# Optimization experiments

Hardware: AMD Instinct MI355X
Metric: run time of the kernel (lower is better)

Reference implementation:

```python
import jax, jax.numpy as jnp
import numpy as np

B, N, IN_DIM, DIM, HEADS = 2, 4096, 1024, 1024, 8
MAX_MASK = 2048
SCALE = DIM ** -0.5  # original uses full dim, not per-head dim


def setup_inputs() -> dict:
    key = jax.random.key(0)
    k_x, k_qkv, k_o, k_b, k_m = jax.random.split(key, 5)
    x = jax.random.normal(k_x, (B, N, IN_DIM), dtype=jnp.float32)
    W_qkv = jax.random.normal(k_qkv, (IN_DIM, 3 * DIM), dtype=jnp.float32) * 0.02
    W_out = jax.random.normal(k_o, (DIM, DIM), dtype=jnp.float32) * 0.02
    b_out = jax.random.normal(k_b, (DIM,), dtype=jnp.float32) * 0.02
    mask = jax.random.randint(k_m, (1, 1, MAX_MASK, MAX_MASK), 0, 2, dtype=jnp.int32)
    return {"x": x, "W_qkv": W_qkv, "W_out": W_out, "b_out": b_out,
            "mask": mask, "max_mask": MAX_MASK}


def reference(x, W_qkv, W_out, b_out, mask, max_mask):
    b, n, _ = x.shape
    d = DIM // HEADS
    qkv = x @ W_qkv                                   # [b, n, 3*dim]
    qkv = qkv.reshape(b, n, 3, HEADS, d).transpose(2, 0, 3, 1, 4)  # [3, b, h, n, d]
    q, k, v = qkv[0], qkv[1], qkv[2]
    dots = jnp.einsum('bhid,bhjd->bhij', q, k) * SCALE  # [b, h, n, n]
    # partial submatrix masking on the top-left [max_mask, max_mask] block
    m = max_mask
    sub = jnp.where(mask == 0, -jnp.inf, dots[:, :, :m, :m])
    dots = dots.at[:, :, :m, :m].set(sub)
    attn = jax.nn.softmax(dots, axis=-1)
    out = jnp.einsum('bhij,bhjd->bhid', attn, v)       # [b, h, n, d]
    out = out.transpose(0, 2, 1, 3).reshape(b, n, HEADS * d)
    return out @ W_out + b_out
```

## Files before the change

kernel.cpp:

```cpp
#include <hip/hip_runtime.h>
#include <hip/hip_bf16.h>
#include <stdint.h>


typedef __attribute__((ext_vector_type(8))) short short8;
typedef __attribute__((ext_vector_type(4))) float f32x4;

#define SCALE_Q 0.03125f

__device__ __forceinline__ unsigned short f2bf(float f) {
  union { float f; unsigned int u; } v;
  v.f = f;
  return (unsigned short)((v.u + 0x7fffu + ((v.u >> 16) & 1u)) >> 16);
}

__device__ __forceinline__ unsigned int pkbf2(float a, float b) {
  __hip_bfloat162 h = __float22bfloat162_rn(make_float2(a, b));
  union { __hip_bfloat162 h; unsigned int u; } c;
  c.h = h;
  return c.u;
}

__device__ __forceinline__ void gload_lds16(const void* g, void* l) {
  __builtin_amdgcn_global_load_lds(
      (const __attribute__((address_space(1))) uint32_t*)(uintptr_t)g,
      (__attribute__((address_space(3))) uint32_t*)(uintptr_t)l, 16, 0, 0);
}

__device__ __forceinline__ f32x4 zero4() {
  f32x4 z; z.x = 0.f; z.y = 0.f; z.z = 0.f; z.w = 0.f; return z;
}

__global__ __launch_bounds__(256) void k_cvt_x(const float* __restrict__ in,
                                               unsigned short* __restrict__ out) {
  const int t = blockIdx.x * 256 + threadIdx.x;
  const float4 v = ((const float4*)in)[t];
  ushort4 o;
  o.x = f2bf(v.x); o.y = f2bf(v.y); o.z = f2bf(v.z); o.w = f2bf(v.w);
  ((ushort4*)out)[t] = o;
}

__global__ __launch_bounds__(256) void k_cvt_wt(const float* __restrict__ w,
                                                unsigned short* __restrict__ wt,
                                                int Nn) {
  __shared__ float t[32][33];
  const int n0 = blockIdx.x << 5, k0 = blockIdx.y << 5;
  const int c = threadIdx.x & 31, r8 = threadIdx.x >> 5;
#pragma unroll
  for (int i = 0; i < 4; ++i) {
    const int r = (i << 3) + r8;
    t[r][c] = w[(long)(k0 + r) * Nn + n0 + c];
  }
  __syncthreads();
#pragma unroll
  for (int i = 0; i < 4; ++i) {
    const int r = (i << 3) + r8;
    wt[(long)(n0 + r) * 1024 + k0 + c] = f2bf(t[c][r]);
  }
}

__global__ __launch_bounds__(256) void k_mask_bits(
    const int* __restrict__ m, unsigned long long* __restrict__ mb) {
  const int t = blockIdx.x * 256 + threadIdx.x;
  const unsigned long long b = __ballot(m[t] != 0);
  if ((threadIdx.x & 63) == 0) mb[t >> 6] = b;
}

__global__ __launch_bounds__(256, 2) void k_qkv_gemm(
    const unsigned short* __restrict__ A,
    const unsigned short* __restrict__ Bt,
    unsigned short* __restrict__ Qs, unsigned short* __restrict__ Ks,
    unsigned short* __restrict__ Vt) {
  __shared__ __align__(16) unsigned short lA[4][128][8];
  __shared__ __align__(16) unsigned short lB[4][128][8];
  const int tid = threadIdx.x;
  const int w = tid >> 6, ln = tid & 63;
  const int m15 = ln & 15, q4 = ln >> 4;
  const int wm = (w >> 1) << 6, wn = (w & 1) << 6;
  const int id = blockIdx.x;
  const int swz = (id & 7) * 192 + (id >> 3);
  const int tn = swz % 24, tm = swz / 24;
  const int which = tn >> 3;
  const int h = tn & 7;

  f32x4 acc[4][4];
#pragma unroll
  for (int i = 0; i < 4; ++i)
#pragma unroll
    for (int j = 0; j < 4; ++j) acc[i][j] = zero4();

  if (which == 2) {
    for (int kb = 0; kb < 1024; kb += 32) {
      __syncthreads();
#pragma unroll
      for (int c = 0; c < 2; ++c) {
        const int p = ((c * 4 + w) << 10) + (ln << 4);
        const int g = p >> 11;
        const int r = (p & 2047) >> 4;
        gload_lds16(A + ((long)tm * 128 + r) * 1024 + kb + g * 8,
                    (char*)&lA[0][0][0] + p);
        gload_lds16(Bt + ((long)tn * 128 + r) * 1024 + kb + g * 8,
                    (char*)&lB[0][0][0] + p);
      }
      __syncthreads();
      short8 afr[4], bfr[4];
#pragma unroll
      for (int i = 0; i < 4; ++i)
        afr[i] = *(const short8*)&lA[q4][wm + i * 16 + m15][0];
#pragma unroll
      for (int j = 0; j < 4; ++j)
        bfr[j] = *(const short8*)&lB[q4][wn + j * 16 + m15][0];
#pragma unroll
      for (int i = 0; i < 4; ++i)
#pragma unroll
        for (int j = 0; j < 4; ++j)
          acc[i][j] = __builtin_amdgcn_mfma_f32_16x16x32_bf16(afr[i], bfr[j],
                                                              acc[i][j], 0, 0, 0);
    }
#pragma unroll
    for (int i = 0; i < 4; ++i) {
      const int m0 = (tm << 7) + wm + (i << 4) + (q4 << 2);
      const int b = m0 >> 12, row0 = m0 & 4095;
#pragma unroll
      for (int j = 0; j < 4; ++j) {
        const int dd = wn + (j << 4) + m15;
        const long bh = b * 8 + h;
        uint2 u;
        u.x = pkbf2(acc[i][j][0], acc[i][j][1]);
        u.y = pkbf2(acc[i][j][2], acc[i][j][3]);
        *(uint2*)&Vt[(bh * 128 + dd) * 4096 + row0] = u;
      }
    }
  } else {
    for (int kb = 0; kb < 1024; kb += 32) {
      __syncthreads();
#pragma unroll
      for (int c = 0; c < 2; ++c) {
        const int p = ((c * 4 + w) << 10) + (ln << 4);
        const int g = p >> 11;
        const int r = (p & 2047) >> 4;
        gload_lds16(A + ((long)tm * 128 + r) * 1024 + kb + g * 8,
                    (char*)&lA[0][0][0] + p);
        gload_lds16(Bt + ((long)tn * 128 + r) * 1024 + kb + g * 8,
                    (char*)&lB[0][0][0] + p);
      }
      __syncthreads();
      short8 afr[4], bfr[4];
#pragma unroll
      for (int i = 0; i < 4; ++i)
        afr[i] = *(const short8*)&lA[q4][wm + i * 16 + m15][0];
#pragma unroll
      for (int j = 0; j < 4; ++j)
        bfr[j] = *(const short8*)&lB[q4][wn + j * 16 + m15][0];
#pragma unroll
      for (int i = 0; i < 4; ++i)
#pragma unroll
        for (int j = 0; j < 4; ++j)
          acc[i][j] = __builtin_amdgcn_mfma_f32_16x16x32_bf16(bfr[j], afr[i],
                                                              acc[i][j], 0, 0, 0);
    }
    unsigned short* Dst = (which == 0) ? Qs : Ks;
    const float sc = (which == 0) ? SCALE_Q : 1.0f;
#pragma unroll
    for (int i = 0; i < 4; ++i) {
      const int m = (tm << 7) + wm + (i << 4) + m15;
      const int b = m >> 12, row = m & 4095;
      const long bh = b * 8 + h;
#pragma unroll
      for (int j = 0; j < 4; ++j) {
        const int dd0 = wn + (j << 4) + (q4 << 2);
        uint2 u;
        u.x = pkbf2(acc[i][j][0] * sc, acc[i][j][1] * sc);
        u.y = pkbf2(acc[i][j][2] * sc, acc[i][j][3] * sc);
        *(uint2*)&Dst[(bh * 4096 + row) * 128 + dd0] = u;
      }
    }
  }
}

__global__ __launch_bounds__(512, 2) void k_flash(
    const unsigned short* __restrict__ Qs, const unsigned short* __restrict__ Ks,
    const unsigned short* __restrict__ Vt,
    const unsigned long long* __restrict__ mbits,
    unsigned short* __restrict__ Ob) {
  __shared__ __align__(16) unsigned short lK[2][16][64][8];
  __shared__ __align__(16) unsigned short lV[2][8][128][8];
  __shared__ __align__(16) unsigned short lP[8][2][16][72];

  const int tid = threadIdx.x;
  const int w = tid >> 6, ln = tid & 63;
  const int m15 = ln & 15, q4 = ln >> 4;
  const int id = blockIdx.x;
  const int xcd = id & 7, jj = id >> 3;
  const int bh = (xcd << 1) | (jj >> 4);
  const int rowblk = jj & 15;
  const int rbase = rowblk * 256 + w * 32;
  const int rq0 = rbase + m15;
  const int rq1 = rbase + 16 + m15;

  const unsigned short* Qbh = Qs + (long)bh * 524288;
  const unsigned short* Kbh = Ks + (long)bh * 524288;
  const unsigned short* Vbh = Vt + (long)bh * 524288;

  short8 qf[2][4];
#pragma unroll
  for (int kk = 0; kk < 4; ++kk) {
    qf[0][kk] = *(const short8*)(Qbh + (long)rq0 * 128 + kk * 32 + q4 * 8);
    qf[1][kk] = *(const short8*)(Qbh + (long)rq1 * 128 + kk * 32 + q4 * 8);
  }

  f32x4 o[2][8];
#pragma unroll
  for (int qg = 0; qg < 2; ++qg)
#pragma unroll
    for (int j = 0; j < 8; ++j) o[qg][j] = zero4();
  f32x4 lacc[2];
  lacc[0] = zero4(); lacc[1] = zero4();

  const bool maskblk = rowblk < 8;

#define STAGE_KV(dst, kvoff)                                              \
  {                                                                       \
    _Pragma("unroll")                                                     \
    for (int c = 0; c < 2; ++c) {                                         \
      const int p = ((c * 8 + w) << 10) + (ln << 4);                      \
      const int cs = p >> 10;                                             \
      const int j = (p & 1023) >> 4;                                      \
      gload_lds16(Kbh + (long)((kvoff) + j) * 128 + cs * 8,               \
                  (char*)&lK[dst][0][0][0] + p);                          \
    }                                                                     \
    _Pragma("unroll")                                                     \
    for (int c = 0; c < 2; ++c) {                                         \
      const int p = ((c * 8 + w) << 10) + (ln << 4);                      \
      const int cv = p >> 11;                                             \
      const int dv = (p & 2047) >> 4;                                     \
      gload_lds16(Vbh + (long)dv * 4096 + (kvoff) + cv * 8,               \
                  (char*)&lV[dst][0][0][0] + p);                          \
    }                                                                     \
  }

  STAGE_KV(0, 0);
  __syncthreads();

  int cur = 0;
  for (int kv = 0; kv < 4096; kv += 64) {
    unsigned long long mw0 = 0ull, mw1 = 0ull;
    const bool domask = maskblk && (kv < 2048);
    if (domask) {
      mw0 = mbits[(long)rq0 * 32 + (kv >> 6)];
      mw1 = mbits[(long)rq1 * 32 + (kv >> 6)];
    }

    const int nb = cur ^ 1;
    if (kv + 64 < 4096) STAGE_KV(nb, kv + 64);

    f32x4 s[2][4];
#pragma unroll
    for (int jt = 0; jt < 4; ++jt) { s[0][jt] = zero4(); s[1][jt] = zero4(); }
    __builtin_amdgcn_s_setprio(1);
#pragma unroll
    for (int jt = 0; jt < 4; ++jt) {
#pragma unroll
      for (int kk = 0; kk < 4; ++kk) {
        const short8 kfr = *(const short8*)&lK[cur][kk * 4 + q4][jt * 16 + m15][0];
        s[0][jt] = __builtin_amdgcn_mfma_f32_16x16x32_bf16(kfr, qf[0][kk],
                                                           s[0][jt], 0, 0, 0);
        s[1][jt] = __builtin_amdgcn_mfma_f32_16x16x32_bf16(kfr, qf[1][kk],
                                                           s[1][jt], 0, 0, 0);
      }
    }
    __builtin_amdgcn_s_setprio(0);

    if (domask) {
#pragma unroll
      for (int jt = 0; jt < 4; ++jt) {
        const unsigned int u0 =
            (jt & 2) ? (unsigned int)(mw0 >> 32) : (unsigned int)mw0;
        const unsigned int u1 =
            (jt & 2) ? (unsigned int)(mw1 >> 32) : (unsigned int)mw1;
        const int base = ((jt & 1) << 4) + (q4 << 2);
#pragma unroll
        for (int r = 0; r < 4; ++r) {
          if (!((u0 >> (base + r)) & 1u)) s[0][jt][r] = -1e30f;
          if (!((u1 >> (base + r)) & 1u)) s[1][jt][r] = -1e30f;
        }
      }
    }

#pragma unroll
    for (int jt = 0; jt < 4; ++jt) {
      f32x4 p0, p1;
      p0.x = __expf(s[0][jt].x); p0.y = __expf(s[0][jt].y);
      p0.z = __expf(s[0][jt].z); p0.w = __expf(s[0][jt].w);
      p1.x = __expf(s[1][jt].x); p1.y = __expf(s[1][jt].y);
      p1.z = __expf(s[1][jt].z); p1.w = __expf(s[1][jt].w);
      lacc[0] += p0; lacc[1] += p1;
      uint2 u0, u1;
      u0.x = pkbf2(p0.x, p0.y); u0.y = pkbf2(p0.z, p0.w);
      u1.x = pkbf2(p1.x, p1.y); u1.y = pkbf2(p1.z, p1.w);
      *(uint2*)&lP[w][0][m15][jt * 16 + q4 * 4] = u0;
      *(uint2*)&lP[w][1][m15][jt * 16 + q4 * 4] = u1;
    }
    __asm__ volatile("s_waitcnt lgkmcnt(0)" ::: "memory");
    __builtin_amdgcn_sched_barrier(0);

    __builtin_amdgcn_s_setprio(1);
#pragma unroll
    for (int kk2 = 0; kk2 < 2; ++kk2) {
      const short8 pf0 = *(const short8*)&lP[w][0][m15][kk2 * 32 + q4 * 8];
      const short8 pf1 = *(const short8*)&lP[w][1][m15][kk2 * 32 + q4 * 8];
#pragma unroll
      for (int jt2 = 0; jt2 < 8; ++jt2) {
        const short8 vf = *(const short8*)&lV[cur][kk2 * 4 + q4][jt2 * 16 + m15][0];
        o[0][jt2] = __builtin_amdgcn_mfma_f32_16x16x32_bf16(pf0, vf,
                                                            o[0][jt2], 0, 0, 0);
        o[1][jt2] = __builtin_amdgcn_mfma_f32_16x16x32_bf16(pf1, vf,
                                                            o[1][jt2], 0, 0, 0);
      }
    }
    __builtin_amdgcn_s_setprio(0);

    __syncthreads();
    cur = nb;
  }
#undef STAGE_KV

  const int b = bh >> 3, h = bh & 7;
#pragma unroll
  for (int qg = 0; qg < 2; ++qg) {
    float lh = lacc[qg].x + lacc[qg].y + lacc[qg].z + lacc[qg].w;
    lh += __shfl_xor(lh, 16);
    lh += __shfl_xor(lh, 32);
    const float linv = 1.0f / lh;
#pragma unroll
    for (int r = 0; r < 4; ++r) {
      const float li = __shfl(linv, q4 * 4 + r);
      const int row = rbase + qg * 16 + q4 * 4 + r;
      unsigned short* op = Ob + ((long)(b * 4096 + row)) * 1024 + h * 128;
#pragma unroll
      for (int jt2 = 0; jt2 < 8; ++jt2)
        op[jt2 * 16 + m15] = f2bf(o[qg][jt2][r] * li);
    }
  }
}

__global__ __launch_bounds__(256, 2) void k_proj_gemm(
    const unsigned short* __restrict__ A,
    const unsigned short* __restrict__ Bt,
    const float* __restrict__ bias, float* __restrict__ Out) {
  __shared__ __align__(16) unsigned short lA[4][128][8];
  __shared__ __align__(16) unsigned short lB[4][128][8];
  const int tid = threadIdx.x;
  const int w = tid >> 6, ln = tid & 63;
  const int m15 = ln & 15, q4 = ln >> 4;
  const int wm = (w >> 1) << 6, wn = (w & 1) << 6;
  const int id = blockIdx.x;
  const int swz = (id & 7) * 64 + (id >> 3);
  const int tn = swz & 7, tm = swz >> 3;

  f32x4 acc[4][4];
#pragma unroll
  for (int i = 0; i < 4; ++i)
#pragma unroll
    for (int j = 0; j < 4; ++j) acc[i][j] = zero4();

  for (int kb = 0; kb < 1024; kb += 32) {
    __syncthreads();
#pragma unroll
    for (int c = 0; c < 2; ++c) {
      const int p = ((c * 4 + w) << 10) + (ln << 4);
      const int g = p >> 11;
      const int r = (p & 2047) >> 4;
      gload_lds16(A + ((long)tm * 128 + r) * 1024 + kb + g * 8,
                  (char*)&lA[0][0][0] + p);
      gload_lds16(Bt + ((long)tn * 128 + r) * 1024 + kb + g * 8,
                  (char*)&lB[0][0][0] + p);
    }
    __syncthreads();
    short8 afr[4], bfr[4];
#pragma unroll
    for (int i = 0; i < 4; ++i)
      afr[i] = *(const short8*)&lA[q4][wm + i * 16 + m15][0];
#pragma unroll
    for (int j = 0; j < 4; ++j)
      bfr[j] = *(const short8*)&lB[q4][wn + j * 16 + m15][0];
#pragma unroll
    for (int i = 0; i < 4; ++i)
#pragma unroll
      for (int j = 0; j < 4; ++j)
        acc[i][j] = __builtin_amdgcn_mfma_f32_16x16x32_bf16(afr[i], bfr[j],
                                                            acc[i][j], 0, 0, 0);
  }

#pragma unroll
  for (int i = 0; i < 4; ++i)
#pragma unroll
    for (int r = 0; r < 4; ++r) {
      const int m = (tm << 7) + wm + (i << 4) + (q4 << 2) + r;
#pragma unroll
      for (int j = 0; j < 4; ++j) {
        const int n = (tn << 7) + wn + (j << 4) + m15;
        Out[(long)m * 1024 + n] = acc[i][j][r] + bias[n];
      }
    }
}

extern "C" void kernel_launch(void* const* d_in, const int* in_sizes, int n_in,
                              void* d_out, int out_size, void* d_ws,
                              size_t ws_size, hipStream_t stream) {
  const float* x = (const float*)d_in[0];
  const float* Wqkv = (const float*)d_in[1];
  const float* Wout = (const float*)d_in[2];
  const float* bout = (const float*)d_in[3];
  const int* mask = (const int*)d_in[4];
  float* out = (float*)d_out;

  char* ws = (char*)d_ws;
  unsigned short* xb     = (unsigned short*)(ws);
  unsigned short* wqkv_t = (unsigned short*)(ws + 16777216);
  unsigned short* wout_t = (unsigned short*)(ws + 23068672);
  unsigned short* Qs     = (unsigned short*)(ws + 25165824);
  unsigned short* Ks     = (unsigned short*)(ws + 41943040);
  unsigned short* Vt     = (unsigned short*)(ws + 58720256);
  unsigned short* Ob     = xb;
  unsigned long long* mbits = (unsigned long long*)wqkv_t;

  hipLaunchKernelGGL(k_cvt_x, dim3(8192), dim3(256), 0, stream, x, xb);
  hipLaunchKernelGGL(k_cvt_wt, dim3(96, 32), dim3(256), 0, stream, Wqkv, wqkv_t, 3072);
  hipLaunchKernelGGL(k_cvt_wt, dim3(32, 32), dim3(256), 0, stream, Wout, wout_t, 1024);
  hipLaunchKernelGGL(k_qkv_gemm, dim3(1536), dim3(256), 0, stream,
                     xb, wqkv_t, Qs, Ks, Vt);
  hipLaunchKernelGGL(k_mask_bits, dim3(16384), dim3(256), 0, stream,
                     mask, mbits);
  hipLaunchKernelGGL(k_flash, dim3(256), dim3(512), 0, stream,
                     Qs, Ks, Vt, mbits, Ob);
  hipLaunchKernelGGL(k_proj_gemm, dim3(512), dim3(256), 0, stream,
                     Ob, wout_t, bout, out);
}
```

Baseline: 434.3 us.

## Use 4 waves with 64 query rows each in flash kernel and exp2 softmax

The flash attention kernel now runs 256 threads per block instead of 512. Each wave handles 64 query rows instead of 32, so every K/V fragment read from LDS feeds four MFMAs rather than two, lowering LDS traffic per FLOP. The Q scale is folded with log2(e) so the kernel can use the native exp2 instruction instead of __expf. The cost is higher register pressure (launch bounds 256,1) and fewer waves per CU to hide latency.

```diff
diff --git a/kernel.cpp b/kernel.cpp
--- a/kernel.cpp
+++ b/kernel.cpp
@@ -6,7 +6,7 @@
 typedef __attribute__((ext_vector_type(8))) short short8;
 typedef __attribute__((ext_vector_type(4))) float f32x4;
 
-#define SCALE_Q 0.03125f
+#define SCALE_Q 0.0450842200f
 
 __device__ __forceinline__ unsigned short f2bf(float f) {
   union { float f; unsigned int u; } v;
@@ -178,14 +178,14 @@
   }
 }
 
-__global__ __launch_bounds__(512, 2) void k_flash(
+__global__ __launch_bounds__(256, 1) void k_flash(
     const unsigned short* __restrict__ Qs, const unsigned short* __restrict__ Ks,
     const unsigned short* __restrict__ Vt,
     const unsigned long long* __restrict__ mbits,
     unsigned short* __restrict__ Ob) {
   __shared__ __align__(16) unsigned short lK[2][16][64][8];
   __shared__ __align__(16) unsigned short lV[2][8][128][8];
-  __shared__ __align__(16) unsigned short lP[8][2][16][72];
+  __shared__ __align__(16) unsigned short lP[4][4][16][72];
 
   const int tid = threadIdx.x;
   const int w = tid >> 6, ln = tid & 63;
@@ -194,44 +194,44 @@
   const int xcd = id & 7, jj = id >> 3;
   const int bh = (xcd << 1) | (jj >> 4);
   const int rowblk = jj & 15;
-  const int rbase = rowblk * 256 + w * 32;
-  const int rq0 = rbase + m15;
-  const int rq1 = rbase + 16 + m15;
+  const int rbase = rowblk * 256 + w * 64;
 
   const unsigned short* Qbh = Qs + (long)bh * 524288;
   const unsigned short* Kbh = Ks + (long)bh * 524288;
   const unsigned short* Vbh = Vt + (long)bh * 524288;
 
-  short8 qf[2][4];
-#pragma unroll
-  for (int kk = 0; kk < 4; ++kk) {
-    qf[0][kk] = *(const short8*)(Qbh + (long)rq0 * 128 + kk * 32 + q4 * 8);
-    qf[1][kk] = *(const short8*)(Qbh + (long)rq1 * 128 + kk * 32 + q4 * 8);
-  }
-
-  f32x4 o[2][8];
-#pragma unroll
-  for (int qg = 0; qg < 2; ++qg)
+  short8 qf[4][4];
+#pragma unroll
+  for (int qg = 0; qg < 4; ++qg)
+#pragma unroll
+    for (int kk = 0; kk < 4; ++kk)
+      qf[qg][kk] = *(const short8*)(Qbh + (long)(rbase + qg * 16 + m15) * 128 +
+                                    kk * 32 + q4 * 8);
+
+  f32x4 o[4][8];
+#pragma unroll
+  for (int qg = 0; qg < 4; ++qg)
 #pragma unroll
     for (int j = 0; j < 8; ++j) o[qg][j] = zero4();
-  f32x4 lacc[2];
-  lacc[0] = zero4(); lacc[1] = zero4();
+  f32x4 lacc[4];
+#pragma unroll
+  for (int qg = 0; qg < 4; ++qg) lacc[qg] = zero4();
 
   const bool maskblk = rowblk < 8;
 
 #define STAGE_KV(dst, kvoff)                                              \
   {                                                                       \
     _Pragma("unroll")                                                     \
-    for (int c = 0; c < 2; ++c) {                                         \
-      const int p = ((c * 8 + w) << 10) + (ln << 4);                      \
+    for (int c = 0; c < 4; ++c) {                                         \
+      const int p = ((c * 4 + w) << 10) + (ln << 4);                      \
       const int cs = p >> 10;                                             \
       const int j = (p & 1023) >> 4;                                      \
       gload_lds16(Kbh + (long)((kvoff) + j) * 128 + cs * 8,               \
                   (char*)&lK[dst][0][0][0] + p);                          \
     }                                                                     \
     _Pragma("unroll")                                                     \
-    for (int c = 0; c < 2; ++c) {                                         \
-      const int p = ((c * 8 + w) << 10) + (ln << 4);                      \
+    for (int c = 0; c < 4; ++c) {                                         \
+      const int p = ((c * 4 + w) << 10) + (ln << 4);                      \
       const int cv = p >> 11;                                             \
       const int dv = (p & 2047) >> 4;                                     \
       gload_lds16(Vbh + (long)dv * 4096 + (kvoff) + cv * 8,               \
@@ -244,62 +244,67 @@
 
   int cur = 0;
   for (int kv = 0; kv < 4096; kv += 64) {
-    unsigned long long mw0 = 0ull, mw1 = 0ull;
+    unsigned long long mw[4];
     const bool domask = maskblk && (kv < 2048);
     if (domask) {
-      mw0 = mbits[(long)rq0 * 32 + (kv >> 6)];
-      mw1 = mbits[(long)rq1 * 32 + (kv >> 6)];
+#pragma unroll
+      for (int qg = 0; qg < 4; ++qg)
+        mw[qg] = mbits[(long)(rbase + qg * 16 + m15) * 32 + (kv >> 6)];
     }
 
     const int nb = cur ^ 1;
     if (kv + 64 < 4096) STAGE_KV(nb, kv + 64);
 
-    f32x4 s[2][4];
-#pragma unroll
-    for (int jt = 0; jt < 4; ++jt) { s[0][jt] = zero4(); s[1][jt] = zero4(); }
+    f32x4 s[4][4];
+#pragma unroll
+    for (int qg = 0; qg < 4; ++qg)
+#pragma unroll
+      for (int jt = 0; jt < 4; ++jt) s[qg][jt] = zero4();
     __builtin_amdgcn_s_setprio(1);
 #pragma unroll
     for (int jt = 0; jt < 4; ++jt) {
 #pragma unroll
       for (int kk = 0; kk < 4; ++kk) {
         const short8 kfr = *(const short8*)&lK[cur][kk * 4 + q4][jt * 16 + m15][0];
-        s[0][jt] = __builtin_amdgcn_mfma_f32_16x16x32_bf16(kfr, qf[0][kk],
-                                                           s[0][jt], 0, 0, 0);
-        s[1][jt] = __builtin_amdgcn_mfma_f32_16x16x32_bf16(kfr, qf[1][kk],
-                                                           s[1][jt], 0, 0, 0);
+#pragma unroll
+        for (int qg = 0; qg < 4; ++qg)
+          s[qg][jt] = __builtin_amdgcn_mfma_f32_16x16x32_bf16(kfr, qf[qg][kk],
+                                                              s[qg][jt], 0, 0, 0);
       }
     }
     __builtin_amdgcn_s_setprio(0);
 
     if (domask) {
 #pragma unroll
+      for (int qg = 0; qg < 4; ++qg) {
+#pragma unroll
+        for (int jt = 0; jt < 4; ++jt) {
+          const unsigned int u =
+              (jt & 2) ? (unsigned int)(mw[qg] >> 32) : (unsigned int)mw[qg];
+          const int base = ((jt & 1) << 4) + (q4 << 2);
+#pragma unroll
+          for (int r = 0; r < 4; ++r) {
+            if (!((u >> (base + r)) & 1u)) s[qg][jt][r] = -1e30f;
+          }
+        }
+      }
+    }
+
+#pragma unroll
+    for (int qg = 0; qg < 4; ++qg) {
+#pragma unroll
       for (int jt = 0; jt < 4; ++jt) {
-        const unsigned int u0 =
-            (jt & 2) ? (unsigned int)(mw0 >> 32) : (unsigned int)mw0;
-        const unsigned int u1 =
-            (jt & 2) ? (unsigned int)(mw1 >> 32) : (unsigned int)mw1;
-        const int base = ((jt & 1) << 4) + (q4 << 2);
-#pragma unroll
-        for (int r = 0; r < 4; ++r) {
-          if (!((u0 >> (base + r)) & 1u)) s[0][jt][r] = -1e30f;
-          if (!((u1 >> (base + r)) & 1u)) s[1][jt][r] = -1e30f;
-        }
-      }
-    }
-
-#pragma unroll
-    for (int jt = 0; jt < 4; ++jt) {
-      f32x4 p0, p1;
-      p0.x = __expf(s[0][jt].x); p0.y = __expf(s[0][jt].y);
-      p0.z = __expf(s[0][jt].z); p0.w = __expf(s[0][jt].w);
-      p1.x = __expf(s[1][jt].x); p1.y = __expf(s[1][jt].y);
-      p1.z = __expf(s[1][jt].z); p1.w = __expf(s[1][jt].w);
-      lacc[0] += p0; lacc[1] += p1;
-      uint2 u0, u1;
-      u0.x = pkbf2(p0.x, p0.y); u0.y = pkbf2(p0.z, p0.w);
-      u1.x = pkbf2(p1.x, p1.y); u1.y = pkbf2(p1.z, p1.w);
-      *(uint2*)&lP[w][0][m15][jt * 16 + q4 * 4] = u0;
-      *(uint2*)&lP[w][1][m15][jt * 16 + q4 * 4] = u1;
+        f32x4 p;
+        p.x = __builtin_amdgcn_exp2f(s[qg][jt].x);
+        p.y = __builtin_amdgcn_exp2f(s[qg][jt].y);
+        p.z = __builtin_amdgcn_exp2f(s[qg][jt].z);
+        p.w = __builtin_amdgcn_exp2f(s[qg][jt].w);
+        lacc[qg] += p;
+        uint2 u;
+        u.x = pkbf2(p.x, p.y);
+        u.y = pkbf2(p.z, p.w);
+        *(uint2*)&lP[w][qg][m15][jt * 16 + q4 * 4] = u;
+      }
     }
     __asm__ volatile("s_waitcnt lgkmcnt(0)" ::: "memory");
     __builtin_amdgcn_sched_barrier(0);
@@ -307,15 +312,17 @@
     __builtin_amdgcn_s_setprio(1);
 #pragma unroll
     for (int kk2 = 0; kk2 < 2; ++kk2) {
-      const short8 pf0 = *(const short8*)&lP[w][0][m15][kk2 * 32 + q4 * 8];
-      const short8 pf1 = *(const short8*)&lP[w][1][m15][kk2 * 32 + q4 * 8];
+      short8 pf[4];
+#pragma unroll
+      for (int qg = 0; qg < 4; ++qg)
+        pf[qg] = *(const short8*)&lP[w][qg][m15][kk2 * 32 + q4 * 8];
 #pragma unroll
       for (int jt2 = 0; jt2 < 8; ++jt2) {
         const short8 vf = *(const short8*)&lV[cur][kk2 * 4 + q4][jt2 * 16 + m15][0];
-        o[0][jt2] = __builtin_amdgcn_mfma_f32_16x16x32_bf16(pf0, vf,
-                                                            o[0][jt2], 0, 0, 0);
-        o[1][jt2] = __builtin_amdgcn_mfma_f32_16x16x32_bf16(pf1, vf,
-                                                            o[1][jt2], 0, 0, 0);
+#pragma unroll
+        for (int qg = 0; qg < 4; ++qg)
+          o[qg][jt2] = __builtin_amdgcn_mfma_f32_16x16x32_bf16(pf[qg], vf,
+                                                               o[qg][jt2], 0, 0, 0);
       }
     }
     __builtin_amdgcn_s_setprio(0);
@@ -327,7 +334,7 @@
 
   const int b = bh >> 3, h = bh & 7;
 #pragma unroll
-  for (int qg = 0; qg < 2; ++qg) {
+  for (int qg = 0; qg < 4; ++qg) {
     float lh = lacc[qg].x + lacc[qg].y + lacc[qg].z + lacc[qg].w;
     lh += __shfl_xor(lh, 16);
     lh += __shfl_xor(lh, 32);
@@ -432,7 +439,7 @@
                      xb, wqkv_t, Qs, Ks, Vt);
   hipLaunchKernelGGL(k_mask_bits, dim3(16384), dim3(256), 0, stream,
                      mask, mbits);
-  hipLaunchKernelGGL(k_flash, dim3(256), dim3(512), 0, stream,
+  hipLaunchKernelGGL(k_flash, dim3(256), dim3(256), 0, stream,
                      Qs, Ks, Vt, mbits, Ob);
   hipLaunchKernelGGL(k_proj_gemm, dim3(512), dim3(256), 0, stream,
                      Ob, wout_t, bout, out);
```

Result: slower. 484.1 us (+11.5%).
